# Kernel tuning notes

Hardware: AMD Instinct MI355X
Metric: run time of the kernel (lower is better)

## Reference

```python
import jax, jax.numpy as jnp
import numpy as np

DIM = 1024
HEADS = 16
HEAD_DIM = DIM // HEADS
HIDDEN = 4 * DIM
EPS = 1e-5
SCALE = HEAD_DIM ** -0.5


def _ln(x, g, b):
    m = jnp.mean(x, axis=-1, keepdims=True)
    v = jnp.mean(jnp.square(x - m), axis=-1, keepdims=True)
    return (x - m) * jax.lax.rsqrt(v + EPS) * g + b


def setup_inputs() -> dict:
    key = jax.random.key(0)
    ks = jax.random.split(key, 12)
    B, L = 4, 1024
    s = lambda fan: 1.0 / np.sqrt(fan)
    return {
        "x": jax.random.normal(ks[0], (B, L, DIM), jnp.float32),
        "skip": jax.random.normal(ks[1], (B, L, DIM), jnp.float32),
        "skip_w": jax.random.normal(ks[2], (2 * DIM, DIM), jnp.float32) * s(2 * DIM),
        "skip_b": jnp.zeros((DIM,), jnp.float32),
        "ln1_g": jnp.ones((DIM,), jnp.float32),
        "ln1_b": jnp.zeros((DIM,), jnp.float32),
        "qkv_w": jax.random.normal(ks[3], (DIM, 3 * DIM), jnp.float32) * s(DIM),
        "proj_w": jax.random.normal(ks[4], (DIM, DIM), jnp.float32) * s(DIM),
        "proj_b": jnp.zeros((DIM,), jnp.float32),
        "ln2_g": jnp.ones((DIM,), jnp.float32),
        "ln2_b": jnp.zeros((DIM,), jnp.float32),
        "fc1_w": jax.random.normal(ks[5], (DIM, HIDDEN), jnp.float32) * s(DIM),
        "fc1_b": jnp.zeros((HIDDEN,), jnp.float32),
        "fc2_w": jax.random.normal(ks[6], (HIDDEN, DIM), jnp.float32) * s(HIDDEN),
        "fc2_b": jnp.zeros((DIM,), jnp.float32),
        "ln3_g": jnp.ones((DIM,), jnp.float32),
        "ln3_b": jnp.zeros((DIM,), jnp.float32),
    }


def reference(x, skip, skip_w, skip_b, ln1_g, ln1_b, qkv_w, proj_w, proj_b,
              ln2_g, ln2_b, fc1_w, fc1_b, fc2_w, fc2_b, ln3_g, ln3_b):
    B, L, C = x.shape
    # skip-concat + linear + norm1
    x = jnp.concatenate([x, skip], axis=2) @ skip_w + skip_b
    x = _ln(x, ln1_g, ln1_b)
    # attention (naive: full [B,H,L,L] score matrix, as in source)
    qkv = (x @ qkv_w).reshape(B, L, 3, HEADS, HEAD_DIM)
    qkv = jnp.transpose(qkv, (2, 0, 3, 1, 4))  # [3,B,H,L,D]
    q, k, v = qkv[0], qkv[1], qkv[2]
    attn = jax.nn.softmax(jnp.einsum("bhld,bhmd->bhlm", q, k) * SCALE, axis=-1)
    o = jnp.einsum("bhlm,bhmd->bhld", attn, v)
    o = jnp.transpose(o, (0, 2, 1, 3)).reshape(B, L, C) @ proj_w + proj_b
    x = x + o
    x = _ln(x, ln2_g, ln2_b)
    # MLP with exact (erf) GELU, matching torch default
    h = jax.nn.gelu(x @ fc1_w + fc1_b, approximate=False)
    x = x + (h @ fc2_w + fc2_b)
    x = _ln(x, ln3_g, ln3_b)
    return x
```

## Files before the change

### kernel.cpp

```cpp
#include <hip/hip_runtime.h>

typedef float f32x4 __attribute__((ext_vector_type(4)));
typedef short s16x8 __attribute__((ext_vector_type(8)));

#define MFMA16(a, b, c) __builtin_amdgcn_mfma_f32_16x16x32_bf16(a, b, c, 0, 0, 0)
#define SCALE 0.125f

__device__ __forceinline__ unsigned short f2bf(float f) {
    unsigned u = __float_as_uint(f);
    u = u + 0x7FFFu + ((u >> 16) & 1u);
    return (unsigned short)(u >> 16);
}

typedef const __attribute__((address_space(1))) void* gptr_t;
typedef __attribute__((address_space(3))) void* lptr_t;
__device__ __forceinline__ void gload16(const void* g, void* l) {
    __builtin_amdgcn_global_load_lds((gptr_t)g, (lptr_t)l, 16, 0, 0);
}

__global__ __launch_bounds__(256) void cvt_cat(const float* __restrict__ x,
                                               const float* __restrict__ skip,
                                               unsigned short* __restrict__ out) {
    const size_t i = ((size_t)blockIdx.x * 256 + threadIdx.x) * 8;
    const int r = (int)(i >> 11);
    const int c = (int)(i & 2047);
    const float* src = (c < 1024) ? (x + (size_t)r * 1024 + c)
                                  : (skip + (size_t)r * 1024 + (c - 1024));
    float4 v0 = *(const float4*)src;
    float4 v1 = *(const float4*)(src + 4);
    s16x8 o;
    o[0] = f2bf(v0.x); o[1] = f2bf(v0.y); o[2] = f2bf(v0.z); o[3] = f2bf(v0.w);
    o[4] = f2bf(v1.x); o[5] = f2bf(v1.y); o[6] = f2bf(v1.z); o[7] = f2bf(v1.w);
    *(s16x8*)(out + i) = o;
}

__global__ __launch_bounds__(256) void wt_tr(const float* __restrict__ in,
                                             unsigned short* __restrict__ out,
                                             int R, int C) {
    __shared__ unsigned short tile[64][72];
    const int nct = C >> 6;
    const int tr = blockIdx.x / nct, tc = blockIdx.x % nct;
    const int t = threadIdx.x;
    const int r = t >> 2, c0 = (t & 3) << 4;
    const float* src = in + (size_t)(tr * 64 + r) * C + tc * 64 + c0;
#pragma unroll
    for (int j = 0; j < 16; j += 4) {
        float4 v = *(const float4*)(src + j);
        tile[r][c0 + j]     = f2bf(v.x);
        tile[r][c0 + j + 1] = f2bf(v.y);
        tile[r][c0 + j + 2] = f2bf(v.z);
        tile[r][c0 + j + 3] = f2bf(v.w);
    }
    __syncthreads();
    const int oc = t >> 2, r0 = (t & 3) << 4;
    s16x8 o0, o1;
#pragma unroll
    for (int j = 0; j < 8; ++j) { o0[j] = tile[r0 + j][oc]; o1[j] = tile[r0 + 8 + j][oc]; }
    unsigned short* dst = out + (size_t)(tc * 64 + oc) * R + tr * 64 + r0;
    *(s16x8*)dst = o0;
    *(s16x8*)(dst + 8) = o1;
}

__global__ __launch_bounds__(256) void v_transpose(const unsigned short* __restrict__ qkv,
                                                   unsigned short* __restrict__ vt) {
    __shared__ unsigned short tile[64][72];
    const int bh = blockIdx.x >> 4, lt = blockIdx.x & 15;
    const int b = bh >> 4, h = bh & 15;
    const int t = threadIdx.x;
    const int r = t >> 2, c0 = (t & 3) << 4;
    const unsigned short* src =
        qkv + (size_t)(b * 1024 + lt * 64 + r) * 3072 + 2048 + h * 64 + c0;
    s16x8 v0 = *(const s16x8*)src;
    s16x8 v1 = *(const s16x8*)(src + 8);
#pragma unroll
    for (int j = 0; j < 8; ++j) { tile[r][c0 + j] = v0[j]; tile[r][c0 + 8 + j] = v1[j]; }
    __syncthreads();
    const int d = t >> 2, l0 = (t & 3) << 4;
    s16x8 o0, o1;
#pragma unroll
    for (int j = 0; j < 8; ++j) { o0[j] = tile[l0 + j][d]; o1[j] = tile[l0 + 8 + j][d]; }
    unsigned short* dst = vt + (size_t)bh * 65536 + (size_t)d * 1024 + lt * 64 + l0;
    *(s16x8*)dst = o0;
    *(s16x8*)(dst + 8) = o1;
}

__global__ __launch_bounds__(256) void ln_kernel(const float* __restrict__ in,
                                                 const float* __restrict__ g,
                                                 const float* __restrict__ bb,
                                                 float* __restrict__ outf,
                                                 unsigned short* __restrict__ outb) {
    const int row = blockIdx.x;
    const int t = threadIdx.x;
    const float4 v = ((const float4*)(in + (size_t)row * 1024))[t];
    float s = v.x + v.y + v.z + v.w;
    float ss = v.x * v.x + v.y * v.y + v.z * v.z + v.w * v.w;
#pragma unroll
    for (int off = 1; off < 64; off <<= 1) {
        s += __shfl_xor(s, off, 64);
        ss += __shfl_xor(ss, off, 64);
    }
    __shared__ float red[8];
    const int wave = t >> 6, lane = t & 63;
    if (lane == 0) { red[wave] = s; red[4 + wave] = ss; }
    __syncthreads();
    s = red[0] + red[1] + red[2] + red[3];
    ss = red[4] + red[5] + red[6] + red[7];
    const float mean = s * 0.0009765625f;
    const float var = ss * 0.0009765625f - mean * mean;
    const float rstd = rsqrtf(var + 1e-5f);
    const float4 gv = ((const float4*)g)[t];
    const float4 bv = ((const float4*)bb)[t];
    float4 ov;
    ov.x = (v.x - mean) * rstd * gv.x + bv.x;
    ov.y = (v.y - mean) * rstd * gv.y + bv.y;
    ov.z = (v.z - mean) * rstd * gv.z + bv.z;
    ov.w = (v.w - mean) * rstd * gv.w + bv.w;
    if (outf) ((float4*)(outf + (size_t)row * 1024))[t] = ov;
    if (outb) {
        ushort4 ob;
        ob.x = f2bf(ov.x); ob.y = f2bf(ov.y); ob.z = f2bf(ov.z); ob.w = f2bf(ov.w);
        *(ushort4*)(outb + (size_t)row * 1024 + t * 4) = ob;
    }
}

template <int EPI>
__global__ __launch_bounds__(256) void gemm_bt(const unsigned short* __restrict__ A,
                                               const unsigned short* __restrict__ Bt,
                                               void* __restrict__ outp,
                                               const float* __restrict__ bias,
                                               const float* __restrict__ resid,
                                               int M, int N, int K) {
    __shared__ __align__(16) unsigned short sA[2][128 * 32];
    __shared__ __align__(16) unsigned short sB[2][128 * 32];
    const int tid = threadIdx.x, wave = tid >> 6, lane = tid & 63;
    const int fr = lane & 15, fq = lane >> 4;
    const int nbn = N >> 7;
    const int bm = blockIdx.x / nbn, bn = blockIdx.x % nbn;
    const int wm = wave >> 1, wn = wave & 1;
    const unsigned short* Ab = A + (size_t)bm * 128 * K;
    const unsigned short* Bb = Bt + (size_t)bn * 128 * K;
    const int srow = wave * 32 + (lane >> 2);
    const int scol = (lane & 3) * 8;

    f32x4 acc[4][4];
#pragma unroll
    for (int i = 0; i < 4; ++i)
#pragma unroll
        for (int j = 0; j < 4; ++j) acc[i][j] = (f32x4){0.f, 0.f, 0.f, 0.f};

    auto stage = [&](int buf, int k0) {
        const unsigned short* ga = Ab + (size_t)srow * K + k0 + scol;
        const unsigned short* gb = Bb + (size_t)srow * K + k0 + scol;
        unsigned short* la = &sA[buf][wave * 32 * 32];
        unsigned short* lb = &sB[buf][wave * 32 * 32];
        gload16(ga, la);
        gload16(ga + (size_t)16 * K, la + 16 * 32);
        gload16(gb, lb);
        gload16(gb + (size_t)16 * K, lb + 16 * 32);
    };

    const int nkt = K >> 5;
    stage(0, 0);
    for (int kt = 0; kt < nkt; ++kt) {
        __syncthreads();
        if (kt + 1 < nkt) stage((kt + 1) & 1, (kt + 1) * 32);
        const unsigned short* a0 = &sA[kt & 1][0];
        const unsigned short* b0 = &sB[kt & 1][0];
        s16x8 af[4], bf[4];
#pragma unroll
        for (int i = 0; i < 4; ++i)
            af[i] = *(const s16x8*)(a0 + (wm * 64 + i * 16 + fr) * 32 + fq * 8);
#pragma unroll
        for (int j = 0; j < 4; ++j)
            bf[j] = *(const s16x8*)(b0 + (wn * 64 + j * 16 + fr) * 32 + fq * 8);
#pragma unroll
        for (int i = 0; i < 4; ++i)
#pragma unroll
            for (int j = 0; j < 4; ++j) acc[i][j] = MFMA16(af[i], bf[j], acc[i][j]);
    }

#pragma unroll
    for (int i = 0; i < 4; ++i) {
        const int row0 = bm * 128 + wm * 64 + i * 16 + fq * 4;
#pragma unroll
        for (int j = 0; j < 4; ++j) {
            const int col = bn * 128 + wn * 64 + j * 16 + fr;
            const float bv = (EPI == 2) ? 0.f : bias[col];
#pragma unroll
            for (int r = 0; r < 4; ++r) {
                const int row = row0 + r;
                float v = acc[i][j][r] + bv;
                if (EPI == 3) v = 0.5f * v * (1.f + erff(v * 0.70710678f));
                if (EPI == 1) v += resid[(size_t)row * N + col];
                if (EPI == 0 || EPI == 1)
                    ((float*)outp)[(size_t)row * N + col] = v;
                else
                    ((unsigned short*)outp)[(size_t)row * N + col] = f2bf(v);
            }
        }
    }
}

__global__ __launch_bounds__(256) void attn_kernel(const unsigned short* __restrict__ qkv,
                                                   const unsigned short* __restrict__ vt,
                                                   unsigned short* __restrict__ o) {
    __shared__ __align__(16) unsigned short sK[2][64 * 64];
    __shared__ __align__(16) unsigned short sV[2][64 * 64];
    __shared__ __align__(16) unsigned short sP[4][16 * 64];

    const int j = blockIdx.x;
    const int xcd = j & 7, ix = j >> 3;
    const int bh = xcd * 8 + (ix >> 4);
    const int qt = ix & 15;
    const int b = bh >> 4, h = bh & 15;

    const int tid = threadIdx.x;
    const int wave = tid >> 6, lane = tid & 63;
    const int fr = lane & 15, fq = lane >> 4;

    const unsigned short* kbase = qkv + (size_t)(b * 1024) * 3072 + 1024 + h * 64;
    const unsigned short* vbase = vt + (size_t)bh * 65536;

    const int qrow0 = b * 1024 + qt * 64 + wave * 16;
    const unsigned short* qp = qkv + (size_t)(qrow0 + fr) * 3072 + h * 64;
    const s16x8 aq0 = *(const s16x8*)(qp + fq * 8);
    const s16x8 aq1 = *(const s16x8*)(qp + 32 + fq * 8);

    const f32x4 zero4 = {0.f, 0.f, 0.f, 0.f};
    float m[4], l[4];
    f32x4 oacc[4];
#pragma unroll
    for (int r = 0; r < 4; ++r) { m[r] = -1e30f; l[r] = 0.f; }
#pragma unroll
    for (int n = 0; n < 4; ++n) oacc[n] = zero4;

    auto stage = [&](int buf, int kt) {
#pragma unroll
        for (int c = 0; c < 2; ++c) {
            const int ob = tid * 16 + c * 4096;
            const int row = ob >> 7;
            const int slot = (ob >> 4) & 7;
            const int cole = ((slot ^ (row & 7)) << 3);
            gload16(kbase + (size_t)(kt * 64 + row) * 3072 + cole,
                    (char*)&sK[buf][0] + ob);
            gload16(vbase + (size_t)row * 1024 + kt * 64 + cole,
                    (char*)&sV[buf][0] + ob);
        }
    };

    unsigned short* pw = &sP[wave][0];
    const int psw = (fr & 7) << 4;

    stage(0, 0);
    for (int kt = 0; kt < 16; ++kt) {
        const int cur = kt & 1;
        __syncthreads();
        if (kt + 1 < 16) stage(cur ^ 1, kt + 1);

        const unsigned short* kb = &sK[cur][0];
        f32x4 s[4];
        __builtin_amdgcn_s_setprio(1);
#pragma unroll
        for (int n = 0; n < 4; ++n) {
            const int R = n * 16 + fr;
            const int sw = (R & 7) << 3;
            const s16x8 bk0 = *(const s16x8*)(kb + R * 64 + ((fq * 8) ^ sw));
            const s16x8 bk1 = *(const s16x8*)(kb + R * 64 + ((32 + fq * 8) ^ sw));
            s[n] = MFMA16(aq0, bk0, zero4);
            s[n] = MFMA16(aq1, bk1, s[n]);
        }
        __builtin_amdgcn_s_setprio(0);

        float mnew[4], alpha[4], rs[4];
#pragma unroll
        for (int r = 0; r < 4; ++r) {
            float t = fmaxf(fmaxf(s[0][r], s[1][r]), fmaxf(s[2][r], s[3][r])) * SCALE;
#pragma unroll
            for (int off = 1; off < 16; off <<= 1) t = fmaxf(t, __shfl_xor(t, off, 64));
            mnew[r] = fmaxf(m[r], t);
            alpha[r] = __expf(m[r] - mnew[r]);
            rs[r] = 0.f;
        }
#pragma unroll
        for (int n = 0; n < 4; ++n) {
#pragma unroll
            for (int r = 0; r < 4; ++r) {
                const float p = __expf(s[n][r] * SCALE - mnew[r]);
                rs[r] += p;
                const int prow = fq * 4 + r;
                const int pb = prow * 128 + (((n * 16 + fr) * 2) ^ ((prow & 7) << 4));
                *(unsigned short*)((char*)pw + pb) = f2bf(p);
            }
        }
#pragma unroll
        for (int r = 0; r < 4; ++r) {
            float t = rs[r];
#pragma unroll
            for (int off = 1; off < 16; off <<= 1) t += __shfl_xor(t, off, 64);
            l[r] = l[r] * alpha[r] + t;
            m[r] = mnew[r];
        }
#pragma unroll
        for (int n = 0; n < 4; ++n) {
            oacc[n][0] *= alpha[0]; oacc[n][1] *= alpha[1];
            oacc[n][2] *= alpha[2]; oacc[n][3] *= alpha[3];
        }

        const s16x8 ap0 = *(const s16x8*)((char*)pw + fr * 128 + ((fq * 16) ^ psw));
        const s16x8 ap1 = *(const s16x8*)((char*)pw + fr * 128 + ((64 + fq * 16) ^ psw));
        const unsigned short* vb = &sV[cur][0];
        __builtin_amdgcn_s_setprio(1);
#pragma unroll
        for (int n = 0; n < 4; ++n) {
            const int R = n * 16 + fr;
            const int sw = (R & 7) << 3;
            const s16x8 bv0 = *(const s16x8*)(vb + R * 64 + ((fq * 8) ^ sw));
            const s16x8 bv1 = *(const s16x8*)(vb + R * 64 + ((32 + fq * 8) ^ sw));
            oacc[n] = MFMA16(ap0, bv0, oacc[n]);
            oacc[n] = MFMA16(ap1, bv1, oacc[n]);
        }
        __builtin_amdgcn_s_setprio(0);
    }

#pragma unroll
    for (int r = 0; r < 4; ++r) {
        const float rl = 1.f / l[r];
        const int row = qrow0 + fq * 4 + r;
#pragma unroll
        for (int n = 0; n < 4; ++n) {
            const int col = h * 64 + n * 16 + fr;
            o[(size_t)row * 1024 + col] = f2bf(oacc[n][r] * rl);
        }
    }
}

extern "C" void kernel_launch(void* const* d_in, const int* in_sizes, int n_in,
                              void* d_out, int out_size, void* d_ws, size_t ws_size,
                              hipStream_t stream) {
    (void)in_sizes; (void)n_in; (void)out_size; (void)ws_size;
    const float* x      = (const float*)d_in[0];
    const float* skip   = (const float*)d_in[1];
    const float* skip_w = (const float*)d_in[2];
    const float* skip_b = (const float*)d_in[3];
    const float* ln1_g  = (const float*)d_in[4];
    const float* ln1_b  = (const float*)d_in[5];
    const float* qkv_w  = (const float*)d_in[6];
    const float* proj_w = (const float*)d_in[7];
    const float* proj_b = (const float*)d_in[8];
    const float* ln2_g  = (const float*)d_in[9];
    const float* ln2_b  = (const float*)d_in[10];
    const float* fc1_w  = (const float*)d_in[11];
    const float* fc1_b  = (const float*)d_in[12];
    const float* fc2_w  = (const float*)d_in[13];
    const float* fc2_b  = (const float*)d_in[14];
    const float* ln3_g  = (const float*)d_in[15];
    const float* ln3_b  = (const float*)d_in[16];

    char* ws = (char*)d_ws;
    const size_t MB = 1u << 20;
    unsigned short* skip_wT = (unsigned short*)(ws + 0 * MB);
    unsigned short* qkv_wT  = (unsigned short*)(ws + 4 * MB);
    unsigned short* proj_wT = (unsigned short*)(ws + 10 * MB);
    unsigned short* fc1_wT  = (unsigned short*)(ws + 12 * MB);
    unsigned short* fc2_wT  = (unsigned short*)(ws + 20 * MB);
    float* pre              = (float*)(ws + 28 * MB);
    float* x1               = (float*)(ws + 44 * MB);
    unsigned short* x1b     = (unsigned short*)(ws + 60 * MB);
    unsigned short* qkvb    = (unsigned short*)(ws + 68 * MB);
    float* x2n              = (float*)(ws + 68 * MB);
    unsigned short* x2nb    = (unsigned short*)(ws + 84 * MB);
    unsigned short* vtb     = (unsigned short*)(ws + 92 * MB);
    unsigned short* ob      = (unsigned short*)(ws + 100 * MB);
    unsigned short* hb      = (unsigned short*)(ws + 108 * MB);
    unsigned short* xcatb   = (unsigned short*)(ws + 108 * MB);
    float* outf = (float*)d_out;

    cvt_cat<<<4096, 256, 0, stream>>>(x, skip, xcatb);
    wt_tr<<<512, 256, 0, stream>>>(skip_w, skip_wT, 2048, 1024);
    wt_tr<<<768, 256, 0, stream>>>(qkv_w, qkv_wT, 1024, 3072);
    wt_tr<<<256, 256, 0, stream>>>(proj_w, proj_wT, 1024, 1024);
    wt_tr<<<1024, 256, 0, stream>>>(fc1_w, fc1_wT, 1024, 4096);
    wt_tr<<<1024, 256, 0, stream>>>(fc2_w, fc2_wT, 4096, 1024);

    gemm_bt<0><<<32 * 8, 256, 0, stream>>>(xcatb, skip_wT, pre, skip_b, nullptr, 4096, 1024, 2048);
    ln_kernel<<<4096, 256, 0, stream>>>(pre, ln1_g, ln1_b, x1, x1b);

    gemm_bt<2><<<32 * 24, 256, 0, stream>>>(x1b, qkv_wT, qkvb, nullptr, nullptr, 4096, 3072, 1024);

    v_transpose<<<1024, 256, 0, stream>>>(qkvb, vtb);
    attn_kernel<<<1024, 256, 0, stream>>>(qkvb, vtb, ob);

    gemm_bt<1><<<32 * 8, 256, 0, stream>>>(ob, proj_wT, pre, proj_b, x1, 4096, 1024, 1024);
    ln_kernel<<<4096, 256, 0, stream>>>(pre, ln2_g, ln2_b, x2n, x2nb);

    gemm_bt<3><<<32 * 32, 256, 0, stream>>>(x2nb, fc1_wT, hb, fc1_b, nullptr, 4096, 4096, 1024);

    gemm_bt<1><<<32 * 8, 256, 0, stream>>>(hb, fc2_wT, pre, fc2_b, x2n, 4096, 1024, 4096);
    ln_kernel<<<4096, 256, 0, stream>>>(pre, ln3_g, ln3_b, outf, nullptr);
}
```

Before: 505.6 us.

## Add 256x256 multi-stage GEMM for QKV and FC1, XCD remap, tanh GELU

Adds a 512-thread GEMM kernel with 256x256 output tiles, a 4-deep LDS ring using direct global-to-LDS loads, explicit vmcnt waits and MFMA priority bumps. It replaces the 128x128 GEMM for the QKV and FC1 projections to raise operand reuse and hide memory latency. Block indices in both GEMMs are remapped so consecutive tiles land on the same XCD for L2 locality. The exact erf GELU is swapped for a tanh-form approximation via exp, which cuts epilogue cost but departs from the exact-erf reference semantics.

```diff
diff --git a/kernel.cpp b/kernel.cpp
--- a/kernel.cpp
+++ b/kernel.cpp
@@ -10,6 +10,13 @@
     unsigned u = __float_as_uint(f);
     u = u + 0x7FFFu + ((u >> 16) & 1u);
     return (unsigned short)(u >> 16);
+}
+
+__device__ __forceinline__ float fast_gelu(float x) {
+    float u = 1.5957691216f * (x + 0.044715f * x * x * x);
+    u = fminf(u, 30.f);
+    const float e = __expf(u);
+    return x * e / (e + 1.f);
 }
 
 typedef const __attribute__((address_space(1))) void* gptr_t;
@@ -135,7 +142,8 @@
     const int tid = threadIdx.x, wave = tid >> 6, lane = tid & 63;
     const int fr = lane & 15, fq = lane >> 4;
     const int nbn = N >> 7;
-    const int bm = blockIdx.x / nbn, bn = blockIdx.x % nbn;
+    const int wg = (blockIdx.x & 7) * ((int)gridDim.x >> 3) + (blockIdx.x >> 3);
+    const int bm = wg / nbn, bn = wg % nbn;
     const int wm = wave >> 1, wn = wave & 1;
     const unsigned short* Ab = A + (size_t)bm * 128 * K;
     const unsigned short* Bb = Bt + (size_t)bn * 128 * K;
@@ -190,12 +198,108 @@
             for (int r = 0; r < 4; ++r) {
                 const int row = row0 + r;
                 float v = acc[i][j][r] + bv;
-                if (EPI == 3) v = 0.5f * v * (1.f + erff(v * 0.70710678f));
+                if (EPI == 3) v = fast_gelu(v);
                 if (EPI == 1) v += resid[(size_t)row * N + col];
                 if (EPI == 0 || EPI == 1)
                     ((float*)outp)[(size_t)row * N + col] = v;
                 else
                     ((unsigned short*)outp)[(size_t)row * N + col] = f2bf(v);
+            }
+        }
+    }
+}
+
+template <int EPI>
+__global__ __launch_bounds__(512) void gemm256(const unsigned short* __restrict__ A,
+                                               const unsigned short* __restrict__ Bt,
+                                               unsigned short* __restrict__ outp,
+                                               const float* __restrict__ bias,
+                                               int N, int K) {
+    __shared__ __align__(16) unsigned short lds[4][16384];
+    const int tid = threadIdx.x, wave = tid >> 6, lane = tid & 63;
+    const int fr = lane & 15, fq = lane >> 4;
+    const int wm = wave >> 2, wn = wave & 3;
+    const int nbn = N >> 8;
+    const int wg = (blockIdx.x & 7) * ((int)gridDim.x >> 3) + (blockIdx.x >> 3);
+    const int bm = wg / nbn, bn = wg % nbn;
+    const unsigned short* Ab = A + (size_t)bm * 256 * K;
+    const unsigned short* Bb = Bt + (size_t)bn * 256 * K;
+    const int nt = K >> 5;
+
+    f32x4 acc[8][4];
+#pragma unroll
+    for (int i = 0; i < 8; ++i)
+#pragma unroll
+        for (int n = 0; n < 4; ++n) acc[i][n] = (f32x4){0.f, 0.f, 0.f, 0.f};
+
+    const int srow = tid >> 2;
+    const int scol = (tid & 3) * 8;
+
+    auto stage2 = [&](int tt, int s0) {
+#pragma unroll
+        for (int s = s0; s < s0 + 2; ++s) {
+            const unsigned short* base = (s < 2) ? Ab : Bb;
+            const int row = ((s & 1) << 7) + srow;
+            gload16(base + (size_t)row * K + tt * 32 + scol,
+                    (char*)&lds[tt & 3][0] + s * 8192 + tid * 16);
+        }
+    };
+
+    stage2(0, 0); stage2(0, 2);
+    stage2(1, 0); stage2(1, 2);
+    stage2(2, 0); stage2(2, 2);
+
+    for (int t = 0; t < nt; ++t) {
+        __builtin_amdgcn_sched_barrier(0);
+        if (t + 2 < nt)      asm volatile("s_waitcnt vmcnt(8)" ::: "memory");
+        else if (t + 1 < nt) asm volatile("s_waitcnt vmcnt(4)" ::: "memory");
+        else                 asm volatile("s_waitcnt vmcnt(0)" ::: "memory");
+        __builtin_amdgcn_sched_barrier(0);
+        __builtin_amdgcn_s_barrier();
+
+        const unsigned short* lb = &lds[t & 3][0];
+        s16x8 af[4], bfr[4];
+#pragma unroll
+        for (int i = 0; i < 4; ++i)
+            af[i] = *(const s16x8*)(lb + (wm * 128 + i * 16 + fr) * 32 + fq * 8);
+#pragma unroll
+        for (int n = 0; n < 4; ++n)
+            bfr[n] = *(const s16x8*)(lb + 8192 + (wn * 64 + n * 16 + fr) * 32 + fq * 8);
+        if (t + 3 < nt) stage2(t + 3, 0);
+        __builtin_amdgcn_s_barrier();
+        __builtin_amdgcn_s_setprio(1);
+#pragma unroll
+        for (int i = 0; i < 4; ++i)
+#pragma unroll
+            for (int n = 0; n < 4; ++n) acc[i][n] = MFMA16(af[i], bfr[n], acc[i][n]);
+        __builtin_amdgcn_s_setprio(0);
+        __builtin_amdgcn_s_barrier();
+#pragma unroll
+        for (int i = 0; i < 4; ++i)
+            af[i] = *(const s16x8*)(lb + (wm * 128 + 64 + i * 16 + fr) * 32 + fq * 8);
+        if (t + 3 < nt) stage2(t + 3, 2);
+        __builtin_amdgcn_s_barrier();
+        __builtin_amdgcn_s_setprio(1);
+#pragma unroll
+        for (int i = 0; i < 4; ++i)
+#pragma unroll
+            for (int n = 0; n < 4; ++n) acc[4 + i][n] = MFMA16(af[i], bfr[n], acc[4 + i][n]);
+        __builtin_amdgcn_s_setprio(0);
+        __builtin_amdgcn_s_barrier();
+    }
+
+#pragma unroll
+    for (int a2 = 0; a2 < 8; ++a2) {
+        const int row0 = bm * 256 + wm * 128 + ((a2 >> 2) << 6) + ((a2 & 3) << 4) + fq * 4;
+#pragma unroll
+        for (int n = 0; n < 4; ++n) {
+            const int col = bn * 256 + wn * 64 + n * 16 + fr;
+            const float bv = (EPI == 3) ? bias[col] : 0.f;
+#pragma unroll
+            for (int r = 0; r < 4; ++r) {
+                float v = acc[a2][n][r] + bv;
+                if (EPI == 3) v = fast_gelu(v);
+                outp[(size_t)(row0 + r) * N + col] = f2bf(v);
             }
         }
     }
@@ -385,7 +489,7 @@
     gemm_bt<0><<<32 * 8, 256, 0, stream>>>(xcatb, skip_wT, pre, skip_b, nullptr, 4096, 1024, 2048);
     ln_kernel<<<4096, 256, 0, stream>>>(pre, ln1_g, ln1_b, x1, x1b);
 
-    gemm_bt<2><<<32 * 24, 256, 0, stream>>>(x1b, qkv_wT, qkvb, nullptr, nullptr, 4096, 3072, 1024);
+    gemm256<2><<<192, 512, 0, stream>>>(x1b, qkv_wT, qkvb, nullptr, 3072, 1024);
 
     v_transpose<<<1024, 256, 0, stream>>>(qkvb, vtb);
     attn_kernel<<<1024, 256, 0, stream>>>(qkvb, vtb, ob);
@@ -393,7 +497,7 @@
     gemm_bt<1><<<32 * 8, 256, 0, stream>>>(ob, proj_wT, pre, proj_b, x1, 4096, 1024, 1024);
     ln_kernel<<<4096, 256, 0, stream>>>(pre, ln2_g, ln2_b, x2n, x2nb);
 
-    gemm_bt<3><<<32 * 32, 256, 0, stream>>>(x2nb, fc1_wT, hb, fc1_b, nullptr, 4096, 4096, 1024);
+    gemm256<3><<<256, 512, 0, stream>>>(x2nb, fc1_wT, hb, fc1_b, 4096, 1024);
 
     gemm_bt<1><<<32 * 8, 256, 0, stream>>>(hb, fc2_wT, pre, fc2_b, x2n, 4096, 1024, 4096);
     ln_kernel<<<4096, 256, 0, stream>>>(pre, ln3_g, ln3_b, outf, nullptr);
```

Result: faster. 491.5 us (-2.8%).
